# Optimization experiments

Hardware: AMD Instinct MI355X
Metric: run time of the kernel (lower is better)

The kernel has to match this reference:

```python
import jax, jax.numpy as jnp
import numpy as np

SEQ, BATCH, IN = 512, 256, 15
H1, H2, FC_HID, NUM_CLASSES = 512, 512, 64, 1


def setup_inputs() -> dict:
    key = jax.random.key(0)
    ks = jax.random.split(key, 14)
    def u(k, shape, fan_in):
        b = 1.0 / np.sqrt(fan_in)
        return jax.random.uniform(k, shape, jnp.float32, -b, b)
    return {
        "x": jax.random.normal(ks[0], (SEQ, BATCH, IN), jnp.float32),
        # PyTorch LSTM params, gate order i,f,g,o stacked along dim 0
        "W_ih1": u(ks[1], (4 * H1, IN), H1),
        "W_hh1": u(ks[2], (4 * H1, H1), H1),
        "b_ih1": u(ks[3], (4 * H1,), H1),
        "b_hh1": u(ks[4], (4 * H1,), H1),
        "W_ih2": u(ks[5], (4 * H2, H1), H2),
        "W_hh2": u(ks[6], (4 * H2, H2), H2),
        "b_ih2": u(ks[7], (4 * H2,), H2),
        "b_hh2": u(ks[8], (4 * H2,), H2),
        "fc1_w": u(ks[9], (FC_HID, H2), H2),
        "fc1_b": u(ks[10], (FC_HID,), H2),
        "fc_w": u(ks[11], (NUM_CLASSES, FC_HID), FC_HID),
        "fc_b": u(ks[12], (NUM_CLASSES,), FC_HID),
    }


def _lstm_cell(x_t, h, c, W_ih, W_hh, b_ih, b_hh):
    # gates: [B, 4H], PyTorch gate order i, f, g, o
    g = x_t @ W_ih.T + b_ih + h @ W_hh.T + b_hh
    i, f, gg, o = jnp.split(g, 4, axis=-1)
    c_new = jax.nn.sigmoid(f) * c + jax.nn.sigmoid(i) * jnp.tanh(gg)
    h_new = jax.nn.sigmoid(o) * jnp.tanh(c_new)
    return h_new, c_new


def reference(x, W_ih1, W_hh1, b_ih1, b_hh1, W_ih2, W_hh2, b_ih2, b_hh2,
              fc1_w, fc1_b, fc_w, fc_b):
    S, B, _ = x.shape
    init = (jnp.zeros((B, H1), x.dtype), jnp.zeros((B, H1), x.dtype),
            jnp.zeros((B, H2), x.dtype), jnp.zeros((B, H2), x.dtype))

    def step(carry, x_t):
        h1, c1, h2, c2 = carry
        h1, c1 = _lstm_cell(x_t, h1, c1, W_ih1, W_hh1, b_ih1, b_hh1)
        h2, c2 = _lstm_cell(h1, h2, c2, W_ih2, W_hh2, b_ih2, b_hh2)
        return (h1, c1, h2, c2), None

    (h1, c1, h2, c2), _ = jax.lax.scan(step, init, x)
    # MLP head on final-timestep top-layer hidden state; `out += out` doubles it
    hn = jax.nn.relu(h2)
    out = jax.nn.relu(hn @ fc1_w.T + fc1_b)
    out = out @ fc_w.T + fc_b
    return out + out
```

## Files before the change

kernel.cpp:

```cpp
#include <hip/hip_runtime.h>
#include <cstdint>
#include <cstddef>

typedef __attribute__((ext_vector_type(8))) short short8;
typedef __attribute__((ext_vector_type(4))) float floatx4;

constexpr int kSeq = 512;
constexpr int kBatch = 256;
constexpr int kIn = 15;
constexpr int kH = 512;
constexpr int kG = 4 * kH;
constexpr int kRing = 17;
constexpr size_t kHSlot = (size_t)kBatch * kH;
constexpr size_t kShmemBytes = 131072 + 4096;

__device__ __forceinline__ unsigned short f2bf(float f) {
    union { float f; unsigned u; } v; v.f = f;
    unsigned u = v.u;
    return (unsigned short)((u + 0x7fffu + ((u >> 16) & 1u)) >> 16);
}

__device__ __forceinline__ float sigm(float x) { return 1.0f / (1.0f + __expf(-x)); }
__device__ __forceinline__ float tanh_(float x) { return 1.0f - 2.0f / (1.0f + __expf(2.0f * x)); }

#define LLC_STORE16(P, V)                                                     \
    asm volatile("global_store_dwordx4 %0, %1, off sc0 sc1"                   \
                 :: "v"(P), "v"(V) : "memory")

__device__ __forceinline__ void waitf(const int* flags, int tgt, int lane, int& fc) {
    if (tgt <= 0) return;
    bool watch = (lane < 32);
    if (__all(!watch || fc >= tgt)) return;
    for (;;) {
        if (watch && fc < tgt)
            fc = __hip_atomic_load(flags + lane,
                                   __ATOMIC_RELAXED, __HIP_MEMORY_SCOPE_AGENT);
        if (__all(!watch || fc >= tgt)) return;
        __builtin_amdgcn_s_sleep(1);
    }
}

__global__ void k_conv(const float* __restrict__ src, unsigned short* __restrict__ dst, int n) {
    int i = blockIdx.x * blockDim.x + threadIdx.x;
    if (i < n) dst[i] = f2bf(src[i]);
}

__global__ void k_conv_pad(const float* __restrict__ src, unsigned short* __restrict__ dst, int rows) {
    int i = blockIdx.x * blockDim.x + threadIdx.x;
    if (i >= rows * 32) return;
    int r = i >> 5, k = i & 31;
    dst[i] = (k < kIn) ? f2bf(src[r * kIn + k]) : (unsigned short)0;
}

__global__ __launch_bounds__(256) void k_persist(
    const unsigned short* __restrict__ whh1b,
    const unsigned short* __restrict__ wih1b,
    const unsigned short* __restrict__ wih2b,
    const unsigned short* __restrict__ whh2b,
    const unsigned short* __restrict__ xb,
    const float* __restrict__ bih1, const float* __restrict__ bhh1,
    const float* __restrict__ bih2, const float* __restrict__ bhh2,
    unsigned short* __restrict__ h1r,
    unsigned short* __restrict__ h2r,
    float* __restrict__ h2f,
    int* __restrict__ flags)
{
    extern __shared__ unsigned short lw[];
    const int bid = blockIdx.x;
    const int g = bid & 3;
    const int role = bid >> 2;
    const bool is2 = role >= 32;
    const int rid = role & 31;
    const int j0 = rid << 4;
    const int tid = (int)threadIdx.x;
    const int wave = tid >> 6;
    const int lane = tid & 63;
    const int lcol = lane & 15;
    const int quad = lane >> 4;
    const int m0 = (g << 6) + wave * 16;
    const int arow = m0 + lcol;
    const int koff = quad * 8;

    int* f1 = flags + g * 1024;
    int* f2 = f1 + 32;
    int* myflag = (is2 ? f2 : f1) + rid;
    unsigned short* scr = lw + 65536 + wave * 384;

    if (!is2) {
        for (int i = tid; i < 4096; i += 256) {
            int ln = i >> 6, gg = ln >> 4, u = ln & 15;
            int c = i & 63, kk = c >> 2, qd = c & 3;
            *(short8*)&lw[((gg * 16 + kk) << 9) + ((qd * 16 + u) << 3)] =
                *(const short8*)&whh1b[(size_t)((gg << 9) + j0 + u) * kH + c * 8];
        }
        for (int i = tid; i < 256; i += 256) {
            int ln = i >> 2, gg = ln >> 4, u = ln & 15;
            int qd = i & 3;
            *(short8*)&lw[((64 + gg) << 9) + ((qd * 16 + u) << 3)] =
                *(const short8*)&wih1b[((gg << 9) + j0 + u) * 32 + qd * 8];
        }
    } else {
        for (int i = tid; i < 4096; i += 256) {
            int ln = i >> 6, gg = ln >> 4, u = ln & 15;
            int c = i & 63, kk = c >> 2, qd = c & 3;
            int dst = ((gg * 16 + kk) << 9) + ((qd * 16 + u) << 3);
            size_t src = (size_t)((gg << 9) + j0 + u) * kH + c * 8;
            *(short8*)&lw[dst] = *(const short8*)&wih2b[src];
            *(short8*)&lw[dst + (64 << 9)] = *(const short8*)&whh2b[src];
        }
    }
    float bsum[4];
#pragma unroll
    for (int gg = 0; gg < 4; ++gg) {
        int n = (gg << 9) + j0 + lcol;
        bsum[gg] = is2 ? (bih2[n] + bhh2[n]) : (bih1[n] + bhh1[n]);
    }
    __syncthreads();

    float creg[4] = {0.f, 0.f, 0.f, 0.f};
    int fc1 = 0, fc2 = 0;

    if (!is2) {
        for (int s = 0; s < kSeq; ++s) {
            if ((s & 15) == 0) {
                if (wave == 0) { waitf(f1, s, lane, fc1); waitf(f2, s, lane, fc2); }
                __syncthreads();
                __builtin_amdgcn_fence(__ATOMIC_ACQUIRE, "agent");
            }
            floatx4 acc[4];
#pragma unroll
            for (int gg = 0; gg < 4; ++gg)
                acc[gg] = (floatx4){bsum[gg], bsum[gg], bsum[gg], bsum[gg]};

            short8 ax = *(const short8*)(xb + ((size_t)s * kBatch + arow) * 32 + koff);

            if (wave == 0) waitf(f1, s, lane, fc1);
            __syncthreads();

            const unsigned short* hp = h1r + (size_t)((s + 16) % kRing) * kHSlot
                                       + (size_t)arow * kH + koff;
            short8 a[16];
#pragma unroll
            for (int kk = 0; kk < 16; ++kk) a[kk] = *(const short8*)(hp + kk * 32);
#pragma unroll
            for (int kk = 0; kk < 16; ++kk) {
#pragma unroll
                for (int gg = 0; gg < 4; ++gg) {
                    short8 b = *(const short8*)&lw[((gg * 16 + kk) << 9) + (lane << 3)];
                    acc[gg] = __builtin_amdgcn_mfma_f32_16x16x32_bf16(a[kk], b, acc[gg], 0, 0, 0);
                }
            }
#pragma unroll
            for (int gg = 0; gg < 4; ++gg) {
                short8 b = *(const short8*)&lw[((64 + gg) << 9) + (lane << 3)];
                acc[gg] = __builtin_amdgcn_mfma_f32_16x16x32_bf16(ax, b, acc[gg], 0, 0, 0);
            }

            unsigned short* hw = h1r + (size_t)(s % kRing) * kHSlot;
#pragma unroll
            for (int r = 0; r < 4; ++r) {
                int row = quad * 4 + r;
                float gi = acc[0][r], gf = acc[1][r], ggv = acc[2][r], go = acc[3][r];
                float cn = sigm(gf) * creg[r] + sigm(gi) * tanh_(ggv);
                float hn = sigm(go) * tanh_(cn);
                creg[r] = cn;
                scr[row * 24 + lcol] = f2bf(hn);
            }
            if (lane < 32) {
                int row = lane >> 1, seg = lane & 1;
                short8 v = *(short8*)&scr[row * 24 + seg * 8];
                unsigned short* gp = hw + (size_t)(m0 + row) * kH + j0 + seg * 8;
                LLC_STORE16(gp, v);
            }
            __builtin_amdgcn_s_waitcnt(0);
            __syncthreads();
            if (tid == 0)
                __hip_atomic_store(myflag, s + 1,
                                   __ATOMIC_RELAXED, __HIP_MEMORY_SCOPE_AGENT);
        }
    } else {
        for (int u = 0; u < kSeq; ++u) {
            if ((u & 15) == 0) {
                if (wave == 0) { waitf(f1, u, lane, fc1); waitf(f2, u, lane, fc2); }
                __syncthreads();
                __builtin_amdgcn_fence(__ATOMIC_ACQUIRE, "agent");
            }
            floatx4 acc[4];
#pragma unroll
            for (int gg = 0; gg < 4; ++gg)
                acc[gg] = (floatx4){bsum[gg], bsum[gg], bsum[gg], bsum[gg]};

            if (wave == 0) waitf(f2, u, lane, fc2);
            __syncthreads();

            const unsigned short* hp2 = h2r + (size_t)((u + 16) % kRing) * kHSlot
                                        + (size_t)arow * kH + koff;
            short8 a[16];
#pragma unroll
            for (int kk = 0; kk < 16; ++kk) a[kk] = *(const short8*)(hp2 + kk * 32);
#pragma unroll
            for (int kk = 0; kk < 16; ++kk) {
#pragma unroll
                for (int gg = 0; gg < 4; ++gg) {
                    short8 b = *(const short8*)&lw[((64 + gg * 16 + kk) << 9) + (lane << 3)];
                    acc[gg] = __builtin_amdgcn_mfma_f32_16x16x32_bf16(a[kk], b, acc[gg], 0, 0, 0);
                }
            }

            if (wave == 0) waitf(f1, u + 1, lane, fc1);
            __syncthreads();

            const unsigned short* hp1 = h1r + (size_t)(u % kRing) * kHSlot
                                        + (size_t)arow * kH + koff;
#pragma unroll
            for (int kk = 0; kk < 16; ++kk) a[kk] = *(const short8*)(hp1 + kk * 32);
#pragma unroll
            for (int kk = 0; kk < 16; ++kk) {
#pragma unroll
                for (int gg = 0; gg < 4; ++gg) {
                    short8 b = *(const short8*)&lw[((gg * 16 + kk) << 9) + (lane << 3)];
                    acc[gg] = __builtin_amdgcn_mfma_f32_16x16x32_bf16(a[kk], b, acc[gg], 0, 0, 0);
                }
            }

            unsigned short* hw = h2r + (size_t)(u % kRing) * kHSlot;
            const int j = j0 + lcol;
#pragma unroll
            for (int r = 0; r < 4; ++r) {
                int row = quad * 4 + r;
                float gi = acc[0][r], gf = acc[1][r], ggv = acc[2][r], go = acc[3][r];
                float cn = sigm(gf) * creg[r] + sigm(gi) * tanh_(ggv);
                float hn = sigm(go) * tanh_(cn);
                creg[r] = cn;
                scr[row * 24 + lcol] = f2bf(hn);
                if (u == kSeq - 1) h2f[(size_t)(m0 + row) * kH + j] = hn;
            }
            if (lane < 32) {
                int row = lane >> 1, seg = lane & 1;
                short8 v = *(short8*)&scr[row * 24 + seg * 8];
                unsigned short* gp = hw + (size_t)(m0 + row) * kH + j0 + seg * 8;
                LLC_STORE16(gp, v);
            }
            __builtin_amdgcn_s_waitcnt(0);
            __syncthreads();
            if (tid == 0)
                __hip_atomic_store(myflag, u + 1,
                                   __ATOMIC_RELAXED, __HIP_MEMORY_SCOPE_AGENT);
        }
    }
}

__global__ __launch_bounds__(64) void k_head(
    const float* __restrict__ h2f, const float* __restrict__ fc1w,
    const float* __restrict__ fc1b, const float* __restrict__ fcw,
    const float* __restrict__ fcb, float* __restrict__ out)
{
    int m = blockIdx.x;
    int j = threadIdx.x;
    const float* hr = h2f + (size_t)m * kH;
    const float* wr = fc1w + (size_t)j * kH;
    float sacc = 0.f;
    for (int k = 0; k < kH; ++k) sacc += fmaxf(hr[k], 0.f) * wr[k];
    float rv = fmaxf(sacc + fc1b[j], 0.f) * fcw[j];
#pragma unroll
    for (int off = 32; off >= 1; off >>= 1) rv += __shfl_down(rv, off);
    if (j == 0) out[m] = 2.0f * (rv + fcb[0]);
}

extern "C" void kernel_launch(void* const* d_in, const int* in_sizes, int n_in,
                              void* d_out, int out_size, void* d_ws, size_t ws_size,
                              hipStream_t stream) {
    const float* x    = (const float*)d_in[0];
    const float* Wih1 = (const float*)d_in[1];
    const float* Whh1 = (const float*)d_in[2];
    const float* bih1 = (const float*)d_in[3];
    const float* bhh1 = (const float*)d_in[4];
    const float* Wih2 = (const float*)d_in[5];
    const float* Whh2 = (const float*)d_in[6];
    const float* bih2 = (const float*)d_in[7];
    const float* bhh2 = (const float*)d_in[8];
    const float* fc1w = (const float*)d_in[9];
    const float* fc1b = (const float*)d_in[10];
    const float* fcw  = (const float*)d_in[11];
    const float* fcb  = (const float*)d_in[12];
    float* out = (float*)d_out;

    char* p = (char*)d_ws;
    auto take = [&](size_t bytes) -> char* {
        char* r = p;
        p += (bytes + 255) & ~(size_t)255;
        return r;
    };
    unsigned short* whh1b = (unsigned short*)take((size_t)kG * kH * 2);
    unsigned short* wih2b = (unsigned short*)take((size_t)kG * kH * 2);
    unsigned short* whh2b = (unsigned short*)take((size_t)kG * kH * 2);
    unsigned short* wih1b = (unsigned short*)take((size_t)kG * 32 * 2);
    unsigned short* xb    = (unsigned short*)take((size_t)kSeq * kBatch * 32 * 2);
    char* state = p;
    unsigned short* h1r = (unsigned short*)take((size_t)kRing * kHSlot * 2);
    unsigned short* h2r = (unsigned short*)take((size_t)kRing * kHSlot * 2);
    int* flags = (int*)take(16384);
    size_t state_bytes = (size_t)((char*)flags + 16384 - state);
    float* h2f = (float*)take((size_t)kBatch * kH * 4);

    hipMemsetAsync(state, 0, state_bytes, stream);

    int n = kG * kH;
    k_conv<<<(n + 255) / 256, 256, 0, stream>>>(Whh1, whh1b, n);
    k_conv<<<(n + 255) / 256, 256, 0, stream>>>(Wih2, wih2b, n);
    k_conv<<<(n + 255) / 256, 256, 0, stream>>>(Whh2, whh2b, n);
    k_conv_pad<<<(kG * 32 + 255) / 256, 256, 0, stream>>>(Wih1, wih1b, kG);
    k_conv_pad<<<(kSeq * kBatch * 32 + 255) / 256, 256, 0, stream>>>(x, xb, kSeq * kBatch);

    hipFuncSetAttribute((const void*)k_persist,
                        hipFuncAttributeMaxDynamicSharedMemorySize, (int)kShmemBytes);
    void* args[] = {&whh1b, &wih1b, &wih2b, &whh2b, &xb,
                    (void*)&bih1, (void*)&bhh1, (void*)&bih2, (void*)&bhh2,
                    &h1r, &h2r, &h2f, &flags};
    hipError_t e = hipLaunchCooperativeKernel((const void*)k_persist, dim3(256), dim3(256),
                                              args, (unsigned)kShmemBytes, stream);
    if (e != hipSuccess) {
        k_persist<<<256, 256, kShmemBytes, stream>>>(
            whh1b, wih1b, wih2b, whh2b, xb, bih1, bhh1, bih2, bhh2,
            h1r, h2r, h2f, flags);
    }

    k_head<<<kBatch, 64, 0, stream>>>(h2f, fc1w, fc1b, fcw, fcb, out);
}
```

Baseline: 4.362 ms.

## Map LSTM roles by XCC id and sync through XCC-local L2 flags

Blocks now read the hardware XCC id and take a dynamic rank from an atomic counter, so that each layer/batch group runs on one XCC. Within that group, hidden-state rings and flags are written with sc0 stores and read with sc0 loads, aiming to keep the exchange in the local L2 instead of the shared LLC. Layer-1 h is also written to a separate LLC-coherent ring for layer 2, and the flags are padded to separate cache lines. Per-wave polling replaces the block-wide wait-then-syncthreads, and a coarse throttle ties layer 1 to layer 2 progress. This depends on the XCC block distribution assumption and uses spin-count timeouts that mark a block dead, which risks silently wrong results if the assumption fails.

```diff
diff --git a/kernel.cpp b/kernel.cpp
--- a/kernel.cpp
+++ b/kernel.cpp
@@ -26,17 +26,44 @@
 #define LLC_STORE16(P, V)                                                     \
     asm volatile("global_store_dwordx4 %0, %1, off sc0 sc1"                   \
                  :: "v"(P), "v"(V) : "memory")
-
-__device__ __forceinline__ void waitf(const int* flags, int tgt, int lane, int& fc) {
-    if (tgt <= 0) return;
-    bool watch = (lane < 32);
-    if (__all(!watch || fc >= tgt)) return;
-    for (;;) {
-        if (watch && fc < tgt)
-            fc = __hip_atomic_load(flags + lane,
-                                   __ATOMIC_RELAXED, __HIP_MEMORY_SCOPE_AGENT);
-        if (__all(!watch || fc >= tgt)) return;
-        __builtin_amdgcn_s_sleep(1);
+#define L2_STORE16(P, V)                                                      \
+    asm volatile("global_store_dwordx4 %0, %1, off sc0"                       \
+                 :: "v"(P), "v"(V) : "memory")
+#define L2_STOREF(P, V)                                                       \
+    asm volatile("global_store_dword %0, %1, off sc0"                         \
+                 :: "v"(P), "v"(V) : "memory")
+
+__device__ __forceinline__ int ld_flag_sc0(const int* p) {
+    int v;
+    asm volatile("global_load_dword %0, %1, off sc0\n\ts_waitcnt vmcnt(0)"
+                 : "=v"(v) : "v"(p) : "memory");
+    return v;
+}
+__device__ __forceinline__ short8 ld16_sc0(const unsigned short* p) {
+    short8 v;
+    asm volatile("global_load_dwordx4 %0, %1, off sc0" : "=v"(v) : "v"(p));
+    return v;
+}
+
+__device__ __forceinline__ void waitq(const int* flags, int tgt, int lane, int& fc, int& dead) {
+    if (tgt <= 0 || dead) return;
+    const int* myf = flags + (lane & 31) * 16;
+    int spin = 0;
+    while (!__all(fc >= tgt)) {
+        if (fc < tgt) fc = ld_flag_sc0(myf);
+        if (++spin > 20000) { dead = 1; return; }
+        if (spin > 4096) __builtin_amdgcn_s_sleep(8);
+    }
+}
+__device__ __forceinline__ void waita(const int* flags, int tgt, int lane, int& fc, int& dead) {
+    if (tgt <= 0 || dead) return;
+    const int* myf = flags + (lane & 31) * 16;
+    int spin = 0;
+    while (!__all(fc >= tgt)) {
+        if (fc < tgt)
+            fc = __hip_atomic_load(myf, __ATOMIC_RELAXED, __HIP_MEMORY_SCOPE_AGENT);
+        if (++spin > 20000) { dead = 1; return; }
+        if (spin > 4096) __builtin_amdgcn_s_sleep(8);
     }
 }
 
@@ -60,31 +87,58 @@
     const unsigned short* __restrict__ xb,
     const float* __restrict__ bih1, const float* __restrict__ bhh1,
     const float* __restrict__ bih2, const float* __restrict__ bhh2,
-    unsigned short* __restrict__ h1r,
-    unsigned short* __restrict__ h2r,
+    unsigned short* __restrict__ h1loc,
+    unsigned short* __restrict__ h1llc,
+    unsigned short* __restrict__ h2loc,
     float* __restrict__ h2f,
-    int* __restrict__ flags)
+    int* __restrict__ flags,
+    int* __restrict__ cnt)
 {
     extern __shared__ unsigned short lw[];
-    const int bid = blockIdx.x;
-    const int g = bid & 3;
-    const int role = bid >> 2;
-    const bool is2 = role >= 32;
-    const int rid = role & 31;
-    const int j0 = rid << 4;
     const int tid = (int)threadIdx.x;
     const int wave = tid >> 6;
     const int lane = tid & 63;
     const int lcol = lane & 15;
     const int quad = lane >> 4;
+
+    unsigned xcc;
+    asm("s_getreg_b32 %0, hwreg(HW_REG_XCC_ID)" : "=s"(xcc));
+    xcc &= 7u;
+    const bool is2 = xcc >= 4;
+    const int g = (int)(xcc & 3u);
+
+    int* ridp = (int*)(lw + 67072);
+    if (tid == 0) *ridp = atomicAdd(cnt + xcc, 1);
+    __syncthreads();
+    const int rid_raw = *ridp;
+    int dead = (rid_raw >= 32) ? 1 : 0;
+    const int rid = rid_raw & 31;
+    const int j0 = rid << 4;
+
     const int m0 = (g << 6) + wave * 16;
     const int arow = m0 + lcol;
     const int koff = quad * 8;
 
-    int* f1 = flags + g * 1024;
-    int* f2 = f1 + 32;
-    int* myflag = (is2 ? f2 : f1) + rid;
+    int* F = flags + g * 4096;
+    int* f1loc = F;
+    int* f2loc = F + 512;
+    int* f1c   = F + 1024;
+    int* uprog = F + 1536;
+    int* myflag = (is2 ? f2loc : f1loc) + rid * 16;
     unsigned short* scr = lw + 65536 + wave * 384;
+
+    {
+        unsigned short* ring = is2 ? h2loc : h1loc;
+        short8 z = (short8){0, 0, 0, 0, 0, 0, 0, 0};
+        if (lane < 32) {
+            int row = lane >> 1, seg = lane & 1;
+            unsigned short* zp = ring + (size_t)16 * kHSlot
+                                 + (size_t)(m0 + row) * kH + j0 + seg * 8;
+            L2_STORE16(zp, z);
+        }
+        if (tid == 0) L2_STOREF(myflag, 0);
+        asm volatile("s_waitcnt vmcnt(0)" ::: "memory");
+    }
 
     if (!is2) {
         for (int i = tid; i < 4096; i += 256) {
@@ -118,14 +172,17 @@
     __syncthreads();
 
     float creg[4] = {0.f, 0.f, 0.f, 0.f};
-    int fc1 = 0, fc2 = 0;
 
     if (!is2) {
+        int fc1 = 0, upc = 0;
         for (int s = 0; s < kSeq; ++s) {
-            if ((s & 15) == 0) {
-                if (wave == 0) { waitf(f1, s, lane, fc1); waitf(f2, s, lane, fc2); }
-                __syncthreads();
-                __builtin_amdgcn_fence(__ATOMIC_ACQUIRE, "agent");
+            if ((s & 3) == 0 && s >= 12 && !dead) {
+                int spin = 0;
+                while (upc < s - 10) {
+                    upc = __hip_atomic_load(uprog, __ATOMIC_RELAXED, __HIP_MEMORY_SCOPE_AGENT);
+                    if (++spin > 20000) { dead = 1; break; }
+                    if (spin > 4096) __builtin_amdgcn_s_sleep(8);
+                }
             }
             floatx4 acc[4];
 #pragma unroll
@@ -134,14 +191,18 @@
 
             short8 ax = *(const short8*)(xb + ((size_t)s * kBatch + arow) * 32 + koff);
 
-            if (wave == 0) waitf(f1, s, lane, fc1);
-            __syncthreads();
-
-            const unsigned short* hp = h1r + (size_t)((s + 16) % kRing) * kHSlot
+            waitq(f1loc, s, lane, fc1, dead);
+            const unsigned short* hp = h1loc + (size_t)((s + 16) % kRing) * kHSlot
                                        + (size_t)arow * kH + koff;
             short8 a[16];
 #pragma unroll
-            for (int kk = 0; kk < 16; ++kk) a[kk] = *(const short8*)(hp + kk * 32);
+            for (int kk = 0; kk < 16; ++kk) a[kk] = ld16_sc0(hp + kk * 32);
+            asm volatile("s_waitcnt vmcnt(0)" ::: "memory");
+            __builtin_amdgcn_sched_barrier(0);
+            __syncthreads();
+            if (tid == 0 && s > 0)
+                __hip_atomic_store(f1c + rid * 16, s,
+                                   __ATOMIC_RELAXED, __HIP_MEMORY_SCOPE_AGENT);
 #pragma unroll
             for (int kk = 0; kk < 16; ++kk) {
 #pragma unroll
@@ -156,12 +217,12 @@
                 acc[gg] = __builtin_amdgcn_mfma_f32_16x16x32_bf16(ax, b, acc[gg], 0, 0, 0);
             }
 
-            unsigned short* hw = h1r + (size_t)(s % kRing) * kHSlot;
+            const size_t sw = (size_t)(s % kRing) * kHSlot;
 #pragma unroll
             for (int r = 0; r < 4; ++r) {
                 int row = quad * 4 + r;
-                float gi = acc[0][r], gf = acc[1][r], ggv = acc[2][r], go = acc[3][r];
-                float cn = sigm(gf) * creg[r] + sigm(gi) * tanh_(ggv);
+                float gi = acc[0][r], gf = acc[1][r], gv = acc[2][r], go = acc[3][r];
+                float cn = sigm(gf) * creg[r] + sigm(gi) * tanh_(gv);
                 float hn = sigm(go) * tanh_(cn);
                 creg[r] = cn;
                 scr[row * 24 + lcol] = f2bf(hn);
@@ -169,35 +230,37 @@
             if (lane < 32) {
                 int row = lane >> 1, seg = lane & 1;
                 short8 v = *(short8*)&scr[row * 24 + seg * 8];
-                unsigned short* gp = hw + (size_t)(m0 + row) * kH + j0 + seg * 8;
-                LLC_STORE16(gp, v);
-            }
-            __builtin_amdgcn_s_waitcnt(0);
+                size_t off = sw + (size_t)(m0 + row) * kH + j0 + seg * 8;
+                L2_STORE16(h1loc + off, v);
+                LLC_STORE16(h1llc + off, v);
+            }
+            asm volatile("s_waitcnt vmcnt(1)" ::: "memory");
             __syncthreads();
-            if (tid == 0)
-                __hip_atomic_store(myflag, s + 1,
-                                   __ATOMIC_RELAXED, __HIP_MEMORY_SCOPE_AGENT);
-        }
+            if (tid == 0) L2_STOREF(f1loc + rid * 16, s + 1);
+        }
+        asm volatile("s_waitcnt vmcnt(0)" ::: "memory");
+        __syncthreads();
+        if (tid == 0)
+            __hip_atomic_store(f1c + rid * 16, kSeq,
+                               __ATOMIC_RELAXED, __HIP_MEMORY_SCOPE_AGENT);
     } else {
+        int fc1 = 0, fc2 = 0;
         for (int u = 0; u < kSeq; ++u) {
-            if ((u & 15) == 0) {
-                if (wave == 0) { waitf(f1, u, lane, fc1); waitf(f2, u, lane, fc2); }
-                __syncthreads();
+            if ((u & 15) == 0)
                 __builtin_amdgcn_fence(__ATOMIC_ACQUIRE, "agent");
-            }
             floatx4 acc[4];
 #pragma unroll
             for (int gg = 0; gg < 4; ++gg)
                 acc[gg] = (floatx4){bsum[gg], bsum[gg], bsum[gg], bsum[gg]};
 
-            if (wave == 0) waitf(f2, u, lane, fc2);
-            __syncthreads();
-
-            const unsigned short* hp2 = h2r + (size_t)((u + 16) % kRing) * kHSlot
+            waitq(f2loc, u, lane, fc2, dead);
+            const unsigned short* hp2 = h2loc + (size_t)((u + 16) % kRing) * kHSlot
                                         + (size_t)arow * kH + koff;
             short8 a[16];
 #pragma unroll
-            for (int kk = 0; kk < 16; ++kk) a[kk] = *(const short8*)(hp2 + kk * 32);
+            for (int kk = 0; kk < 16; ++kk) a[kk] = ld16_sc0(hp2 + kk * 32);
+            asm volatile("s_waitcnt vmcnt(0)" ::: "memory");
+            __builtin_amdgcn_sched_barrier(0);
 #pragma unroll
             for (int kk = 0; kk < 16; ++kk) {
 #pragma unroll
@@ -207,13 +270,13 @@
                 }
             }
 
-            if (wave == 0) waitf(f1, u + 1, lane, fc1);
-            __syncthreads();
-
-            const unsigned short* hp1 = h1r + (size_t)(u % kRing) * kHSlot
+            waita(f1c, u + 1, lane, fc1, dead);
+            const unsigned short* hp1 = h1llc + (size_t)(u % kRing) * kHSlot
                                         + (size_t)arow * kH + koff;
 #pragma unroll
-            for (int kk = 0; kk < 16; ++kk) a[kk] = *(const short8*)(hp1 + kk * 32);
+            for (int kk = 0; kk < 16; ++kk) a[kk] = ld16_sc0(hp1 + kk * 32);
+            asm volatile("s_waitcnt vmcnt(0)" ::: "memory");
+            __builtin_amdgcn_sched_barrier(0);
 #pragma unroll
             for (int kk = 0; kk < 16; ++kk) {
 #pragma unroll
@@ -223,13 +286,13 @@
                 }
             }
 
-            unsigned short* hw = h2r + (size_t)(u % kRing) * kHSlot;
+            const size_t sw = (size_t)(u % kRing) * kHSlot;
             const int j = j0 + lcol;
 #pragma unroll
             for (int r = 0; r < 4; ++r) {
                 int row = quad * 4 + r;
-                float gi = acc[0][r], gf = acc[1][r], ggv = acc[2][r], go = acc[3][r];
-                float cn = sigm(gf) * creg[r] + sigm(gi) * tanh_(ggv);
+                float gi = acc[0][r], gf = acc[1][r], gv = acc[2][r], go = acc[3][r];
+                float cn = sigm(gf) * creg[r] + sigm(gi) * tanh_(gv);
                 float hn = sigm(go) * tanh_(cn);
                 creg[r] = cn;
                 scr[row * 24 + lcol] = f2bf(hn);
@@ -238,14 +301,17 @@
             if (lane < 32) {
                 int row = lane >> 1, seg = lane & 1;
                 short8 v = *(short8*)&scr[row * 24 + seg * 8];
-                unsigned short* gp = hw + (size_t)(m0 + row) * kH + j0 + seg * 8;
-                LLC_STORE16(gp, v);
-            }
-            __builtin_amdgcn_s_waitcnt(0);
+                size_t off = sw + (size_t)(m0 + row) * kH + j0 + seg * 8;
+                L2_STORE16(h2loc + off, v);
+            }
+            asm volatile("s_waitcnt vmcnt(0)" ::: "memory");
             __syncthreads();
-            if (tid == 0)
-                __hip_atomic_store(myflag, u + 1,
-                                   __ATOMIC_RELAXED, __HIP_MEMORY_SCOPE_AGENT);
+            if (tid == 0) {
+                L2_STOREF(f2loc + rid * 16, u + 1);
+                if (rid == 0)
+                    __hip_atomic_store(uprog, u + 1,
+                                       __ATOMIC_RELAXED, __HIP_MEMORY_SCOPE_AGENT);
+            }
         }
     }
 }
@@ -297,10 +363,12 @@
     unsigned short* wih1b = (unsigned short*)take((size_t)kG * 32 * 2);
     unsigned short* xb    = (unsigned short*)take((size_t)kSeq * kBatch * 32 * 2);
     char* state = p;
-    unsigned short* h1r = (unsigned short*)take((size_t)kRing * kHSlot * 2);
-    unsigned short* h2r = (unsigned short*)take((size_t)kRing * kHSlot * 2);
-    int* flags = (int*)take(16384);
-    size_t state_bytes = (size_t)((char*)flags + 16384 - state);
+    unsigned short* h1loc = (unsigned short*)take((size_t)kRing * kHSlot * 2);
+    unsigned short* h1llc = (unsigned short*)take((size_t)kRing * kHSlot * 2);
+    unsigned short* h2loc = (unsigned short*)take((size_t)kRing * kHSlot * 2);
+    int* flags = (int*)take(65536);
+    int* cnt   = (int*)take(256);
+    size_t state_bytes = (size_t)((char*)cnt + 256 - state);
     float* h2f = (float*)take((size_t)kBatch * kH * 4);
 
     hipMemsetAsync(state, 0, state_bytes, stream);
@@ -316,13 +384,13 @@
                         hipFuncAttributeMaxDynamicSharedMemorySize, (int)kShmemBytes);
     void* args[] = {&whh1b, &wih1b, &wih2b, &whh2b, &xb,
                     (void*)&bih1, (void*)&bhh1, (void*)&bih2, (void*)&bhh2,
-                    &h1r, &h2r, &h2f, &flags};
+                    &h1loc, &h1llc, &h2loc, &h2f, &flags, &cnt};
     hipError_t e = hipLaunchCooperativeKernel((const void*)k_persist, dim3(256), dim3(256),
                                               args, (unsigned)kShmemBytes, stream);
     if (e != hipSuccess) {
         k_persist<<<256, 256, kShmemBytes, stream>>>(
             whh1b, wih1b, wih2b, whh2b, xb, bih1, bhh1, bih2, bhh2,
-            h1r, h2r, h2f, flags);
+            h1loc, h1llc, h2loc, h2f, flags, cnt);
     }
 
     k_head<<<kBatch, 64, 0, stream>>>(h2f, fc1w, fc1b, fcw, fcb, out);
```

After: 8.246 ms. +89.0%, slower.
